# Kernel optimization log

Hardware: AMD Instinct MI355X
Metric: run time of the kernel (lower is better)

## Reference

```python
import jax, jax.numpy as jnp
import numpy as np

B, N = 16, 128
DN0, DE0, DH = 64, 16, 128  # input node dim, input edge dim, hidden dim


def _gnn2(A, x, e, w_msg, b_msg, w_node, b_node):
    """One GNN2 layer on dense batched graphs.
    A: [B,N,N] adjacency mask, x: [B,N,Dn], e: [B,N,N,De].
    Message/new-edge: relu(Linear([x_i, x_j, e_ij])) masked by A.
    New node: relu(Linear([x, sum_j msg_ij])).
    The concat-Linear is decomposed into three matmuls to avoid
    materializing the [B,N,N,2Dn+De] concat tensor.
    """
    Dn = x.shape[-1]
    Wi, Wj, We = w_msg[:Dn], w_msg[Dn:2 * Dn], w_msg[2 * Dn:]
    xi = x @ Wi                                   # [B,N,Do]
    xj = x @ Wj                                   # [B,N,Do]
    msg = jax.nn.relu(xi[:, :, None, :] + xj[:, None, :, :] + e @ We + b_msg)
    msg = msg * A[..., None]                      # mask non-edges -> new edge_attr [B,N,N,Do]
    agg = msg.sum(axis=2)                         # scatter-sum over neighbors j -> [B,N,Do]
    Wx, Wa = w_node[:Dn], w_node[Dn:]
    x_new = jax.nn.relu(x @ Wx + agg @ Wa + b_node)
    return x_new, msg


def setup_inputs() -> dict:
    key = jax.random.key(0)
    ks = iter(jax.random.split(key, 32))
    s = 0.05
    inp = {
        "edge_index": jax.random.randint(next(ks), (B, N, N), 0, 2, dtype=jnp.int32),
        "x": jax.random.normal(next(ks), (B, N, DN0), dtype=jnp.float32),
        "edge_attr": jax.random.normal(next(ks), (B, N, N, DE0), dtype=jnp.float32),
    }
    def w(shape):
        return s * jax.random.normal(next(ks), shape, dtype=jnp.float32)
    # layer 0: node_in=64, edge_in=16 -> 128
    inp["w_msg_0"], inp["b_msg_0"] = w((2 * DN0 + DE0, DH)), w((DH,))
    inp["w_node_0"], inp["b_node_0"] = w((DN0 + DH, DH)), w((DH,))
    # layers 1,2: 128 -> 128
    for l in (1, 2):
        inp[f"w_msg_{l}"], inp[f"b_msg_{l}"] = w((2 * DH + DH, DH)), w((DH,))
        inp[f"w_node_{l}"], inp[f"b_node_{l}"] = w((DH + DH, DH)), w((DH,))
    # head mlp: 128 -> 128 -> 128 -> 1
    inp["w_h1"], inp["b_h1"] = w((DH, DH)), w((DH,))
    inp["w_h2"], inp["b_h2"] = w((DH, DH)), w((DH,))
    inp["w_h3"], inp["b_h3"] = w((DH, 1)), w((1,))
    return inp


def reference(edge_index, x, edge_attr,
              w_msg_0, b_msg_0, w_node_0, b_node_0,
              w_msg_1, b_msg_1, w_node_1, b_node_1,
              w_msg_2, b_msg_2, w_node_2, b_node_2,
              w_h1, b_h1, w_h2, b_h2, w_h3, b_h3):
    A = edge_index.astype(jnp.float32)
    x = x.astype(jnp.float32)
    # layer 0
    x, e = _gnn2(A, x, edge_attr, w_msg_0, b_msg_0, w_node_0, b_node_0)
    # middle layer with 0.5 residual blend
    x_, e_ = _gnn2(A, x, e, w_msg_1, b_msg_1, w_node_1, b_node_1)
    x = 0.5 * (x + x_)
    e = 0.5 * (e + e_)
    # last layer
    x, e = _gnn2(A, x, e, w_msg_2, b_msg_2, w_node_2, b_node_2)
    # edge_mean readout + MLP head
    h = e.mean(axis=(1, 2))                       # [B, DH]
    h = jax.nn.relu(h @ w_h1 + b_h1)
    h = jax.nn.relu(h @ w_h2 + b_h2)
    out = h @ w_h3 + b_h3                         # [B, 1]
    return out.squeeze(-1)                        # [B]
```

## Files before the change

### kernel.cpp

```cpp
#include <hip/hip_runtime.h>

constexpr int B = 16, N = 128, D = 128, DN0 = 64, DE0 = 16;

typedef _Float16 half8 __attribute__((ext_vector_type(8)));
typedef _Float16 half4 __attribute__((ext_vector_type(4)));
typedef float floatx4 __attribute__((ext_vector_type(4)));
typedef float floatx16 __attribute__((ext_vector_type(16)));

__device__ __forceinline__ void gld16(const _Float16* g, _Float16* l) {
  __builtin_amdgcn_global_load_lds(
      (const __attribute__((address_space(1))) void*)g,
      (__attribute__((address_space(3))) void*)l, 16, 0, 0);
}

__global__ __launch_bounds__(128) void k_wprep(
    const float* __restrict__ wm1, const float* __restrict__ wm2,
    _Float16* __restrict__ weT1, _Float16* __restrict__ weT2) {
  const int bid = blockIdx.x;
  const int layer = bid >> 7, c = bid & 127;
  const int k = threadIdx.x;
  const float* src = layer ? wm2 : wm1;
  _Float16* dst = layer ? weT2 : weT1;
  dst[c * D + k] = (_Float16)src[(2 * D + k) * D + c];
}

__global__ __launch_bounds__(128) void k_pre0(
    const float* __restrict__ x, const float* __restrict__ wm0,
    const float* __restrict__ bm0,
    float* __restrict__ xi0, float* __restrict__ xj0) {
  const int row = blockIdx.x;
  const int c = threadIdx.x;
  __shared__ float xr[DN0];
  if (c < DN0) xr[c] = x[row * DN0 + c];
  __syncthreads();
  float ai = bm0[c], aj = 0.f;
  #pragma unroll 8
  for (int k = 0; k < DN0; ++k) {
    const float xv = xr[k];
    ai = fmaf(xv, wm0[k * D + c], ai);
    aj = fmaf(xv, wm0[(DN0 + k) * D + c], aj);
  }
  xi0[row * D + c] = ai;
  xj0[row * D + c] = aj;
}

__global__ __launch_bounds__(256) void k_edge0(
    const int* __restrict__ ei, const float* __restrict__ eattr,
    const float* __restrict__ wm0,
    const float* __restrict__ xi0, const float* __restrict__ xj0,
    _Float16* __restrict__ msg0, float* __restrict__ agg0) {
  const int row = blockIdx.x;
  const int b = row >> 7;
  const int t = threadIdx.x;
  const int c4 = (t & 31) * 4, jb = t >> 5;

  __shared__ float e_row[N][20];
  __shared__ float w_t[DE0][D];
  __shared__ float amask[N];
  __shared__ float xi_r[D];
  __shared__ float hp2[8][32][4];

  const float4* esrc = (const float4*)(eattr + (size_t)row * N * DE0);
  const float4* wsrc = (const float4*)(wm0 + 2 * DN0 * D);
  #pragma unroll
  for (int u = 0; u < 2; ++u) {
    const int idx4 = u * 256 + t;
    const int j = idx4 >> 2;
    const int k4 = (idx4 & 3) * 4;
    *(float4*)&e_row[j][k4] = esrc[idx4];
    ((float4*)&w_t[0][0])[idx4] = wsrc[idx4];
  }
  if (t < N) {
    amask[t] = (float)ei[(size_t)row * N + t];
    xi_r[t] = xi0[row * D + t];
  }
  __syncthreads();

  float acc[16][4] = {};
  #pragma unroll 4
  for (int k = 0; k < DE0; ++k) {
    float av[16];
    #pragma unroll
    for (int p = 0; p < 16; ++p) av[p] = e_row[jb + 8 * p][k];
    const floatx4 wv = *(const floatx4*)&w_t[k][c4];
    #pragma unroll
    for (int p = 0; p < 16; ++p)
      #pragma unroll
      for (int q = 0; q < 4; ++q)
        acc[p][q] = fmaf(av[p], wv[q], acc[p][q]);
  }

  float hq[4] = {};
  const float* xjb = xj0 + (size_t)b * N * D;
  _Float16* mrow = msg0 + (size_t)row * N * D;
  const floatx4 xiv = *(const floatx4*)&xi_r[c4];
  #pragma unroll
  for (int p = 0; p < 16; ++p) {
    const int j = jb + 8 * p;
    const float am = amask[j];
    const floatx4 xjv = *(const floatx4*)&xjb[j * D + c4];
    half4 hv;
    #pragma unroll
    for (int q = 0; q < 4; ++q) {
      float v = xiv[q] + xjv[q] + acc[p][q];
      v = fmaxf(v, 0.f) * am;
      hv[q] = (_Float16)v;
      hq[q] += v;
    }
    const int cell = (c4 >> 3) ^ (j & 15);
    *(half4*)&mrow[j * D + cell * 8 + (c4 & 7)] = hv;
  }
  #pragma unroll
  for (int q = 0; q < 4; ++q) hp2[jb][t & 31][q] = hq[q];
  __syncthreads();
  if (t < D) {
    float s = 0.f;
    #pragma unroll
    for (int g = 0; g < 8; ++g) s += hp2[g][t >> 2][t & 3];
    agg0[row * D + t] = s;
  }
}

__global__ __launch_bounds__(128) void k_node0(
    const float* __restrict__ x0, const float* __restrict__ agg0,
    const float* __restrict__ wn0, const float* __restrict__ bn0,
    const float* __restrict__ wm1, const float* __restrict__ bm1,
    float* __restrict__ x1, float* __restrict__ xi1, float* __restrict__ xj1) {
  const int row = blockIdx.x;
  const int c = threadIdx.x;
  __shared__ float xr[DN0], ar[D], x1r[D];
  if (c < DN0) xr[c] = x0[row * DN0 + c];
  ar[c] = agg0[row * D + c];
  __syncthreads();
  float a = bn0[c];
  #pragma unroll 8
  for (int k = 0; k < DN0; ++k) a = fmaf(xr[k], wn0[k * D + c], a);
  #pragma unroll 8
  for (int k = 0; k < D; ++k) a = fmaf(ar[k], wn0[(DN0 + k) * D + c], a);
  a = fmaxf(a, 0.f);
  x1[row * D + c] = a;
  x1r[c] = a;
  __syncthreads();
  float ai = bm1[c], aj = 0.f;
  #pragma unroll 8
  for (int k = 0; k < D; ++k) {
    const float xv = x1r[k];
    ai = fmaf(xv, wm1[k * D + c], ai);
    aj = fmaf(xv, wm1[(D + k) * D + c], aj);
  }
  xi1[row * D + c] = ai;
  xj1[row * D + c] = aj;
}

__global__ __launch_bounds__(128) void k_node1(
    const float* __restrict__ x1, const float* __restrict__ agg1,
    const float* __restrict__ wn1, const float* __restrict__ bn1,
    const float* __restrict__ wm2, const float* __restrict__ bm2,
    float* __restrict__ xi2, float* __restrict__ xj2) {
  const int row = blockIdx.x;
  const int c = threadIdx.x;
  __shared__ float x1r[D], ar[D], x2r[D];
  x1r[c] = x1[row * D + c];
  ar[c] = agg1[row * D + c];
  __syncthreads();
  float a = bn1[c];
  #pragma unroll 8
  for (int k = 0; k < D; ++k) a = fmaf(x1r[k], wn1[k * D + c], a);
  #pragma unroll 8
  for (int k = 0; k < D; ++k) a = fmaf(ar[k], wn1[(D + k) * D + c], a);
  x2r[c] = 0.5f * (x1r[c] + fmaxf(a, 0.f));
  __syncthreads();
  float ai = bm2[c], aj = 0.f;
  #pragma unroll 8
  for (int k = 0; k < D; ++k) {
    const float xv = x2r[k];
    ai = fmaf(xv, wm2[k * D + c], ai);
    aj = fmaf(xv, wm2[(D + k) * D + c], aj);
  }
  xi2[row * D + c] = ai;
  xj2[row * D + c] = aj;
}

__global__ __launch_bounds__(256, 2) void k_mid(
    const int* __restrict__ ei, const _Float16* __restrict__ weT1,
    const _Float16* __restrict__ weT2,
    const float* __restrict__ xi, const float* __restrict__ xj,
    _Float16* __restrict__ em,
    float* __restrict__ agg1) {
  const int row = blockIdx.x;
  const int b = row >> 7;
  const int t = threadIdx.x;
  const int w = t >> 6;
  const int lane = t & 63;
  const int l31 = lane & 31;
  const int l15 = lane & 15;
  const int hl = lane >> 5;

  __shared__ _Float16 sE[N * D];

  const _Float16* gsrc = em + (size_t)row * N * D;
  #pragma unroll
  for (int u = 0; u < 8; ++u) {
    const int seg = (u * 4 + w) * 512;
    gld16(gsrc + seg + lane * 8, &sE[seg]);
  }

  half8 a1[8];
  #pragma unroll
  for (int ks = 0; ks < 8; ++ks)
    a1[ks] = *(const half8*)(weT1 + (32 * w + l31) * D + 16 * ks + 8 * hl);

  floatx4 xiv[4];
  #pragma unroll
  for (int g = 0; g < 4; ++g)
    xiv[g] = *(const floatx4*)&xi[(size_t)row * D + 32 * w + 8 * g + 4 * hl];
  float am[4];
  #pragma unroll
  for (int jt = 0; jt < 4; ++jt)
    am[jt] = (float)ei[(size_t)row * N + 32 * jt + l31];

  __syncthreads();

  const floatx16 vzero = {0.f,0.f,0.f,0.f,0.f,0.f,0.f,0.f,
                          0.f,0.f,0.f,0.f,0.f,0.f,0.f,0.f};
  floatx16 acc[4];
  #pragma unroll
  for (int jt = 0; jt < 4; ++jt) acc[jt] = vzero;
  #pragma unroll
  for (int ks = 0; ks < 8; ++ks)
    #pragma unroll
    for (int jt = 0; jt < 4; ++jt) {
      const half8 bv = *(const half8*)
          &sE[(32 * jt + l31) * D + (((2 * ks + hl) ^ l15) << 3)];
      acc[jt] = __builtin_amdgcn_mfma_f32_32x32x16_f16(a1[ks], bv, acc[jt], 0, 0, 0);
    }

  __syncthreads();

  const float* xjb = xj + (size_t)b * N * D;
  floatx4 hacc[4];
  #pragma unroll
  for (int g = 0; g < 4; ++g) hacc[g] = (floatx4){0.f, 0.f, 0.f, 0.f};
  #pragma unroll
  for (int jt = 0; jt < 4; ++jt) {
    const int j = 32 * jt + l31;
    #pragma unroll
    for (int g = 0; g < 4; ++g) {
      const int cofs = 32 * w + 8 * g + 4 * hl;
      const int hidx = j * D + (((4 * w + g) ^ l15) << 3) + 4 * hl;
      const floatx4 xjv = *(const floatx4*)&xjb[j * D + cofs];
      const half4 m0 = *(const half4*)&sE[hidx];
      half4 mid;
      floatx4 m1;
      #pragma unroll
      for (int r = 0; r < 4; ++r) {
        const float v = xiv[g][r] + xjv[r] + acc[jt][4 * g + r];
        m1[r] = fmaxf(v, 0.f) * am[jt];
        mid[r] = (_Float16)(0.5f * ((float)m0[r] + m1[r]));
      }
      *(half4*)&sE[hidx] = mid;
      hacc[g] += m1;
    }
  }

  #pragma unroll
  for (int m = 1; m < 32; m <<= 1)
    #pragma unroll
    for (int g = 0; g < 4; ++g)
      #pragma unroll
      for (int r = 0; r < 4; ++r)
        hacc[g][r] += __shfl_xor(hacc[g][r], m, 64);
  if (l31 == 0) {
    #pragma unroll
    for (int g = 0; g < 4; ++g)
      *(floatx4*)&agg1[(size_t)row * D + 32 * w + 8 * g + 4 * hl] = hacc[g];
  }

  half8 a2[8];
  #pragma unroll
  for (int ks = 0; ks < 8; ++ks)
    a2[ks] = *(const half8*)(weT2 + (32 * w + l31) * D + 16 * ks + 8 * hl);

  __syncthreads();

  #pragma unroll
  for (int jt = 0; jt < 4; ++jt) acc[jt] = vzero;
  #pragma unroll
  for (int ks = 0; ks < 8; ++ks)
    #pragma unroll
    for (int jt = 0; jt < 4; ++jt) {
      const half8 bv = *(const half8*)
          &sE[(32 * jt + l31) * D + (((2 * ks + hl) ^ l15) << 3)];
      acc[jt] = __builtin_amdgcn_mfma_f32_32x32x16_f16(a2[ks], bv, acc[jt], 0, 0, 0);
    }

  __syncthreads();

  #pragma unroll
  for (int jt = 0; jt < 4; ++jt) {
    const int j = 32 * jt + l31;
    #pragma unroll
    for (int g = 0; g < 4; ++g) {
      const int hidx = j * D + (((4 * w + g) ^ l15) << 3) + 4 * hl;
      half4 tv;
      #pragma unroll
      for (int r = 0; r < 4; ++r) tv[r] = (_Float16)acc[jt][4 * g + r];
      *(half4*)&sE[hidx] = tv;
    }
  }

  __syncthreads();

  uint4* gdst = (uint4*)(em + (size_t)row * N * D);
  const uint4* ls = (const uint4*)sE;
  #pragma unroll
  for (int u = 0; u < 8; ++u) {
    const int idx4 = u * 256 + t;
    gdst[idx4] = ls[idx4];
  }
}

__global__ __launch_bounds__(256) void k_fin(
    const int* __restrict__ ei, const _Float16* __restrict__ t2,
    const float* __restrict__ xi, const float* __restrict__ xj,
    float* __restrict__ rowsum) {
  const int row = blockIdx.x;
  const int b = row >> 7;
  const int t = threadIdx.x;
  const int c8 = (t & 15) * 8, jr = t >> 4;

  __shared__ float sMask[N];
  __shared__ float hp[16][16][8];
  if (t < N) sMask[t] = (float)ei[(size_t)row * N + t];
  float xiv[8];
  *(floatx4*)&xiv[0] = *(const floatx4*)&xi[row * D + c8];
  *(floatx4*)&xiv[4] = *(const floatx4*)&xi[row * D + c8 + 4];
  __syncthreads();

  const _Float16* src = t2 + (size_t)row * N * D;
  const float* xjb = xj + (size_t)b * N * D;
  float acc8[8] = {};
  #pragma unroll
  for (int u = 0; u < 8; ++u) {
    const int j = u * 16 + jr;
    const half8 tv = *(const half8*)(src + j * D + (((t & 15) ^ jr) << 3));
    const float am = sMask[j];
    const floatx4 xj0 = *(const floatx4*)&xjb[j * D + c8];
    const floatx4 xj1 = *(const floatx4*)&xjb[j * D + c8 + 4];
    #pragma unroll
    for (int r = 0; r < 4; ++r) {
      acc8[r]     += fmaxf(xiv[r] + xj0[r] + (float)tv[r], 0.f) * am;
      acc8[4 + r] += fmaxf(xiv[4 + r] + xj1[r] + (float)tv[4 + r], 0.f) * am;
    }
  }
  #pragma unroll
  for (int k = 0; k < 8; ++k) hp[jr][t & 15][k] = acc8[k];
  __syncthreads();
  if (t < D) {
    float s = 0.f;
    #pragma unroll
    for (int g = 0; g < 16; ++g) s += hp[g][t >> 3][t & 7];
    rowsum[row * D + t] = s;
  }
}

__global__ __launch_bounds__(128) void k_head(
    const float* __restrict__ rowsum,
    const float* __restrict__ w1, const float* __restrict__ b1,
    const float* __restrict__ w2, const float* __restrict__ b2,
    const float* __restrict__ w3, const float* __restrict__ b3,
    float* __restrict__ out) {
  const int b = blockIdx.x;
  const int c = threadIdx.x;
  __shared__ float hr[D], h1r[D], h2r[D];
  const float* rs = rowsum + (size_t)b * N * D;
  float s = 0.f;
  for (int i = 0; i < N; ++i) s += rs[i * D + c];
  hr[c] = s * (1.f / (N * N));
  __syncthreads();
  float a = b1[c];
  #pragma unroll 8
  for (int k = 0; k < D; ++k) a = fmaf(hr[k], w1[k * D + c], a);
  h1r[c] = fmaxf(a, 0.f);
  __syncthreads();
  a = b2[c];
  #pragma unroll 8
  for (int k = 0; k < D; ++k) a = fmaf(h1r[k], w2[k * D + c], a);
  h2r[c] = fmaxf(a, 0.f);
  __syncthreads();
  hr[c] = h2r[c] * w3[c];
  __syncthreads();
  if (c == 0) {
    float s2 = b3[0];
    for (int k = 0; k < D; ++k) s2 += hr[k];
    out[b] = s2;
  }
}

extern "C" void kernel_launch(void* const* d_in, const int* in_sizes, int n_in,
                              void* d_out, int out_size, void* d_ws, size_t ws_size,
                              hipStream_t stream) {
  const int*   ei  = (const int*)d_in[0];
  const float* x0  = (const float*)d_in[1];
  const float* ea  = (const float*)d_in[2];
  const float* wm0 = (const float*)d_in[3];
  const float* bm0 = (const float*)d_in[4];
  const float* wn0 = (const float*)d_in[5];
  const float* bn0 = (const float*)d_in[6];
  const float* wm1 = (const float*)d_in[7];
  const float* bm1 = (const float*)d_in[8];
  const float* wn1 = (const float*)d_in[9];
  const float* bn1 = (const float*)d_in[10];
  const float* wm2 = (const float*)d_in[11];
  const float* bm2 = (const float*)d_in[12];
  const float* wh1 = (const float*)d_in[15];
  const float* bh1 = (const float*)d_in[16];
  const float* wh2 = (const float*)d_in[17];
  const float* bh2 = (const float*)d_in[18];
  const float* wh3 = (const float*)d_in[19];
  const float* bh3 = (const float*)d_in[20];
  float* out = (float*)d_out;

  _Float16* msg0h = (_Float16*)d_ws;
  _Float16* weT1  = msg0h + (size_t)B * N * N * D;
  _Float16* weT2  = weT1 + D * D;
  float* f = (float*)(weT2 + D * D);
  size_t off = 0;
  const size_t R = (size_t)B * N * D;
  float* xi0  = f + off; off += R;
  float* xj0  = f + off; off += R;
  float* agg0 = f + off; off += R;
  float* x1   = f + off; off += R;
  float* xi1  = f + off; off += R;
  float* xj1  = f + off; off += R;
  float* agg1 = f + off; off += R;
  float* xi2  = f + off; off += R;
  float* xj2  = f + off; off += R;
  float* rsum = f + off; off += R;

  const int rows = B * N;
  k_wprep<<<256, 128, 0, stream>>>(wm1, wm2, weT1, weT2);
  k_pre0 <<<rows, 128, 0, stream>>>(x0, wm0, bm0, xi0, xj0);
  k_edge0<<<rows, 256, 0, stream>>>(ei, ea, wm0, xi0, xj0, msg0h, agg0);
  k_node0<<<rows, 128, 0, stream>>>(x0, agg0, wn0, bn0, wm1, bm1, x1, xi1, xj1);
  k_mid  <<<rows, 256, 0, stream>>>(ei, weT1, weT2, xi1, xj1, msg0h, agg1);
  k_node1<<<rows, 128, 0, stream>>>(x1, agg1, wn1, bn1, wm2, bm2, xi2, xj2);
  k_fin  <<<rows, 256, 0, stream>>>(ei, msg0h, xi2, xj2, rsum);
  k_head <<<B,    128, 0, stream>>>(rsum, wh1, bh1, wh2, bh2, wh3, bh3, out);
}
```

Baseline: 239.4 us.

## Fuse node-update kernels into edge0 and mid kernels, keeping aggregates in LDS

Removes the separate k_node0 and k_node1 launches by running the per-row node update and next-layer xi/xj projection as a tail of k_edge0 and k_mid, with the aggregate kept in shared memory instead of round-tripping through global agg buffers. This cuts two kernel launches and the related global traffic. In exchange, those tail phases use only half the threads of each block and extend block lifetime. k_mid's launch bound is also raised from 2 to 4 blocks per CU, which may increase register pressure or spills.

```diff
diff --git a/kernel.cpp b/kernel.cpp
--- a/kernel.cpp
+++ b/kernel.cpp
@@ -46,9 +46,12 @@
 
 __global__ __launch_bounds__(256) void k_edge0(
     const int* __restrict__ ei, const float* __restrict__ eattr,
-    const float* __restrict__ wm0,
+    const float* __restrict__ wm0, const float* __restrict__ x0,
     const float* __restrict__ xi0, const float* __restrict__ xj0,
-    _Float16* __restrict__ msg0, float* __restrict__ agg0) {
+    const float* __restrict__ wn0, const float* __restrict__ bn0,
+    const float* __restrict__ wm1, const float* __restrict__ bm1,
+    _Float16* __restrict__ msg0, float* __restrict__ x1,
+    float* __restrict__ xi1, float* __restrict__ xj1) {
   const int row = blockIdx.x;
   const int b = row >> 7;
   const int t = threadIdx.x;
@@ -59,6 +62,7 @@
   __shared__ float amask[N];
   __shared__ float xi_r[D];
   __shared__ float hp2[8][32][4];
+  __shared__ float sX0[DN0], sAgg[D], sX1[D];
 
   const float4* esrc = (const float4*)(eattr + (size_t)row * N * DE0);
   const float4* wsrc = (const float4*)(wm0 + 2 * DN0 * D);
@@ -73,6 +77,8 @@
   if (t < N) {
     amask[t] = (float)ei[(size_t)row * N + t];
     xi_r[t] = xi0[row * D + t];
+  } else if (t < N + DN0) {
+    sX0[t - N] = x0[(size_t)row * DN0 + (t - N)];
   }
   __syncthreads();
 
@@ -117,76 +123,45 @@
     float s = 0.f;
     #pragma unroll
     for (int g = 0; g < 8; ++g) s += hp2[g][t >> 2][t & 3];
-    agg0[row * D + t] = s;
-  }
-}
-
-__global__ __launch_bounds__(128) void k_node0(
-    const float* __restrict__ x0, const float* __restrict__ agg0,
-    const float* __restrict__ wn0, const float* __restrict__ bn0,
-    const float* __restrict__ wm1, const float* __restrict__ bm1,
-    float* __restrict__ x1, float* __restrict__ xi1, float* __restrict__ xj1) {
-  const int row = blockIdx.x;
-  const int c = threadIdx.x;
-  __shared__ float xr[DN0], ar[D], x1r[D];
-  if (c < DN0) xr[c] = x0[row * DN0 + c];
-  ar[c] = agg0[row * D + c];
-  __syncthreads();
-  float a = bn0[c];
-  #pragma unroll 8
-  for (int k = 0; k < DN0; ++k) a = fmaf(xr[k], wn0[k * D + c], a);
-  #pragma unroll 8
-  for (int k = 0; k < D; ++k) a = fmaf(ar[k], wn0[(DN0 + k) * D + c], a);
-  a = fmaxf(a, 0.f);
-  x1[row * D + c] = a;
-  x1r[c] = a;
-  __syncthreads();
-  float ai = bm1[c], aj = 0.f;
-  #pragma unroll 8
-  for (int k = 0; k < D; ++k) {
-    const float xv = x1r[k];
-    ai = fmaf(xv, wm1[k * D + c], ai);
-    aj = fmaf(xv, wm1[(D + k) * D + c], aj);
-  }
-  xi1[row * D + c] = ai;
-  xj1[row * D + c] = aj;
-}
-
-__global__ __launch_bounds__(128) void k_node1(
-    const float* __restrict__ x1, const float* __restrict__ agg1,
-    const float* __restrict__ wn1, const float* __restrict__ bn1,
-    const float* __restrict__ wm2, const float* __restrict__ bm2,
-    float* __restrict__ xi2, float* __restrict__ xj2) {
-  const int row = blockIdx.x;
-  const int c = threadIdx.x;
-  __shared__ float x1r[D], ar[D], x2r[D];
-  x1r[c] = x1[row * D + c];
-  ar[c] = agg1[row * D + c];
-  __syncthreads();
-  float a = bn1[c];
-  #pragma unroll 8
-  for (int k = 0; k < D; ++k) a = fmaf(x1r[k], wn1[k * D + c], a);
-  #pragma unroll 8
-  for (int k = 0; k < D; ++k) a = fmaf(ar[k], wn1[(D + k) * D + c], a);
-  x2r[c] = 0.5f * (x1r[c] + fmaxf(a, 0.f));
-  __syncthreads();
-  float ai = bm2[c], aj = 0.f;
-  #pragma unroll 8
-  for (int k = 0; k < D; ++k) {
-    const float xv = x2r[k];
-    ai = fmaf(xv, wm2[k * D + c], ai);
-    aj = fmaf(xv, wm2[(D + k) * D + c], aj);
-  }
-  xi2[row * D + c] = ai;
-  xj2[row * D + c] = aj;
-}
-
-__global__ __launch_bounds__(256, 2) void k_mid(
+    sAgg[t] = s;
+  }
+  __syncthreads();
+
+  if (t < D) {
+    const int c = t;
+    float a = bn0[c];
+    #pragma unroll 8
+    for (int k = 0; k < DN0; ++k) a = fmaf(sX0[k], wn0[k * D + c], a);
+    #pragma unroll 8
+    for (int k = 0; k < D; ++k) a = fmaf(sAgg[k], wn0[(DN0 + k) * D + c], a);
+    a = fmaxf(a, 0.f);
+    x1[(size_t)row * D + c] = a;
+    sX1[c] = a;
+  }
+  __syncthreads();
+  if (t < D) {
+    const int c = t;
+    float ai = bm1[c], aj = 0.f;
+    #pragma unroll 8
+    for (int k = 0; k < D; ++k) {
+      const float xv = sX1[k];
+      ai = fmaf(xv, wm1[k * D + c], ai);
+      aj = fmaf(xv, wm1[(D + k) * D + c], aj);
+    }
+    xi1[(size_t)row * D + c] = ai;
+    xj1[(size_t)row * D + c] = aj;
+  }
+}
+
+__global__ __launch_bounds__(256, 4) void k_mid(
     const int* __restrict__ ei, const _Float16* __restrict__ weT1,
     const _Float16* __restrict__ weT2,
     const float* __restrict__ xi, const float* __restrict__ xj,
+    const float* __restrict__ x1,
+    const float* __restrict__ wn1, const float* __restrict__ bn1,
+    const float* __restrict__ wm2, const float* __restrict__ bm2,
     _Float16* __restrict__ em,
-    float* __restrict__ agg1) {
+    float* __restrict__ xi2, float* __restrict__ xj2) {
   const int row = blockIdx.x;
   const int b = row >> 7;
   const int t = threadIdx.x;
@@ -197,6 +172,7 @@
   const int hl = lane >> 5;
 
   __shared__ _Float16 sE[N * D];
+  __shared__ float sAgg[D], sX1[D], sX2[D];
 
   const _Float16* gsrc = em + (size_t)row * N * D;
   #pragma unroll
@@ -218,6 +194,7 @@
   #pragma unroll
   for (int jt = 0; jt < 4; ++jt)
     am[jt] = (float)ei[(size_t)row * N + 32 * jt + l31];
+  if (t < D) sX1[t] = x1[(size_t)row * D + t];
 
   __syncthreads();
 
@@ -273,7 +250,7 @@
   if (l31 == 0) {
     #pragma unroll
     for (int g = 0; g < 4; ++g)
-      *(floatx4*)&agg1[(size_t)row * D + 32 * w + 8 * g + 4 * hl] = hacc[g];
+      *(floatx4*)&sAgg[32 * w + 8 * g + 4 * hl] = hacc[g];
   }
 
   half8 a2[8];
@@ -317,6 +294,29 @@
   for (int u = 0; u < 8; ++u) {
     const int idx4 = u * 256 + t;
     gdst[idx4] = ls[idx4];
+  }
+
+  if (t < D) {
+    const int c = t;
+    float a = bn1[c];
+    #pragma unroll 8
+    for (int k = 0; k < D; ++k) a = fmaf(sX1[k], wn1[k * D + c], a);
+    #pragma unroll 8
+    for (int k = 0; k < D; ++k) a = fmaf(sAgg[k], wn1[(D + k) * D + c], a);
+    sX2[c] = 0.5f * (sX1[c] + fmaxf(a, 0.f));
+  }
+  __syncthreads();
+  if (t < D) {
+    const int c = t;
+    float ai = bm2[c], aj = 0.f;
+    #pragma unroll 8
+    for (int k = 0; k < D; ++k) {
+      const float xv = sX2[k];
+      ai = fmaf(xv, wm2[k * D + c], ai);
+      aj = fmaf(xv, wm2[(D + k) * D + c], aj);
+    }
+    xi2[(size_t)row * D + c] = ai;
+    xj2[(size_t)row * D + c] = aj;
   }
 }
 
@@ -429,11 +429,9 @@
   const size_t R = (size_t)B * N * D;
   float* xi0  = f + off; off += R;
   float* xj0  = f + off; off += R;
-  float* agg0 = f + off; off += R;
   float* x1   = f + off; off += R;
   float* xi1  = f + off; off += R;
   float* xj1  = f + off; off += R;
-  float* agg1 = f + off; off += R;
   float* xi2  = f + off; off += R;
   float* xj2  = f + off; off += R;
   float* rsum = f + off; off += R;
@@ -441,10 +439,12 @@
   const int rows = B * N;
   k_wprep<<<256, 128, 0, stream>>>(wm1, wm2, weT1, weT2);
   k_pre0 <<<rows, 128, 0, stream>>>(x0, wm0, bm0, xi0, xj0);
-  k_edge0<<<rows, 256, 0, stream>>>(ei, ea, wm0, xi0, xj0, msg0h, agg0);
-  k_node0<<<rows, 128, 0, stream>>>(x0, agg0, wn0, bn0, wm1, bm1, x1, xi1, xj1);
-  k_mid  <<<rows, 256, 0, stream>>>(ei, weT1, weT2, xi1, xj1, msg0h, agg1);
-  k_node1<<<rows, 128, 0, stream>>>(x1, agg1, wn1, bn1, wm2, bm2, xi2, xj2);
+  k_edge0<<<rows, 256, 0, stream>>>(ei, ea, wm0, x0, xi0, xj0,
+                                    wn0, bn0, wm1, bm1,
+                                    msg0h, x1, xi1, xj1);
+  k_mid  <<<rows, 256, 0, stream>>>(ei, weT1, weT2, xi1, xj1, x1,
+                                    wn1, bn1, wm2, bm2,
+                                    msg0h, xi2, xj2);
   k_fin  <<<rows, 256, 0, stream>>>(ei, msg0h, xi2, xj2, rsum);
   k_head <<<B,    128, 0, stream>>>(rsum, wh1, bh1, wh2, bh2, wh3, bh3, out);
 }
```

After: 261.5 us. 9.3% more time.
